# Kernel tuning notes

Hardware: AMD Instinct MI355X
Metric: run time of the kernel (lower is better)

Reference implementation:

```python
import jax, jax.numpy as jnp
import numpy as np

H = 128       # hidden size
IN = 6        # input size
OUT = 1       # output size
B, T = 128, 2048


def setup_inputs() -> dict:
    key = jax.random.key(0)
    ks = jax.random.split(key, 16)
    s = 1.0 / np.sqrt(H)  # PyTorch LSTM init: U(-1/sqrt(H), 1/sqrt(H))
    u = lambda k, shape: jax.random.uniform(k, shape, jnp.float32, -s, s)
    inp = {"x": jax.random.normal(ks[0], (B, T, IN), jnp.float32)}
    in_sizes = [IN, H, H]
    for l in range(3):
        inp[f"W_ih{l}"] = u(ks[1 + 4 * l], (4 * H, in_sizes[l]))
        inp[f"W_hh{l}"] = u(ks[2 + 4 * l], (4 * H, H))
        inp[f"b_ih{l}"] = u(ks[3 + 4 * l], (4 * H,))
        inp[f"b_hh{l}"] = u(ks[4 + 4 * l], (4 * H,))
    inp["W_out"] = u(ks[13], (OUT, H))
    inp["b_out"] = u(ks[14], (OUT,))
    return inp


def _lstm_layer(x, W_ih, W_hh, b):
    # x: [B, T, D_in]; precompute input contribution once, scan the recurrence.
    xg = jnp.einsum("bti,gi->btg", x, W_ih) + b  # [B, T, 4H]
    h0 = jnp.zeros((x.shape[0], H), x.dtype)
    c0 = jnp.zeros((x.shape[0], H), x.dtype)

    def step(carry, xg_t):
        h, c = carry
        g = xg_t + h @ W_hh.T                     # [B, 4H]
        i, f, gg, o = jnp.split(g, 4, axis=-1)    # PyTorch gate order i,f,g,o
        i = jax.nn.sigmoid(i)
        f = jax.nn.sigmoid(f)
        gg = jnp.tanh(gg)
        o = jax.nn.sigmoid(o)
        c = f * c + i * gg
        h = o * jnp.tanh(c)
        return (h, c), h

    _, hs = jax.lax.scan(step, (h0, c0), jnp.swapaxes(xg, 0, 1))  # hs: [T, B, H]
    return jnp.swapaxes(hs, 0, 1)


def reference(x, W_ih0, W_hh0, b_ih0, b_hh0, W_ih1, W_hh1, b_ih1, b_hh1,
              W_ih2, W_hh2, b_ih2, b_hh2, W_out, b_out):
    # 3-layer LSTM (dropout inactive in eval mode) + linear head on last step.
    h = _lstm_layer(x, W_ih0, W_hh0, b_ih0 + b_hh0)
    h = _lstm_layer(h, W_ih1, W_hh1, b_ih1 + b_hh1)
    h = _lstm_layer(h, W_ih2, W_hh2, b_ih2 + b_hh2)
    return h[:, -1, :] @ W_out.T + b_out  # [B, 1]
```

## Files before the change

### kernel.cpp

```cpp
#include <hip/hip_runtime.h>

#define B_ 128
#define T_ 2048
#define H_ 128
#define IN_ 6
#define GRP_ 8
#define NGRP_ (T_ / GRP_)
#define CHUNK_ 32
#define NCHUNK_ (T_ / CHUNK_)
#define FLAG_STRIDE_ 64
#define HS_ 144
#define XGRING_ 3
#define XGSLOT_ (CHUNK_ * 8192)
#define NSLICE_ 32
#define NFLAGS_ 144

typedef _Float16 f16x8 __attribute__((ext_vector_type(8)));
typedef float    f32x4 __attribute__((ext_vector_type(4)));

__device__ __forceinline__ unsigned short f2h_u(float f) {
  union { _Float16 h; unsigned short u; } v; v.h = (_Float16)f; return v.u;
}
__device__ __forceinline__ unsigned int pack2(float a, float b) {
  return (unsigned int)f2h_u(a) | ((unsigned int)f2h_u(b) << 16);
}
__device__ __forceinline__ float sigf_(float x) {
  return __builtin_amdgcn_rcpf(1.0f + __expf(-x));
}
__device__ __forceinline__ float tanhf_(float x) {
  return 2.0f * __builtin_amdgcn_rcpf(1.0f + __expf(-2.0f * x)) - 1.0f;
}
__device__ __forceinline__ f16x8 load_w8(const float* __restrict__ p) {
  f16x8 r;
#pragma unroll
  for (int i = 0; i < 8; ++i) r[i] = (_Float16)p[i];
  return r;
}

__global__ void init_flags(unsigned int* flags) {
  flags[blockIdx.x * 256 + threadIdx.x] = 0u;
}

#define BARRIER_LGKM()                                              \
  do {                                                              \
    asm volatile("s_waitcnt lgkmcnt(0)" ::: "memory");              \
    __builtin_amdgcn_s_barrier();                                   \
    __builtin_amdgcn_sched_barrier(0);                              \
  } while (0)

#define PUBLISH_FENCE()                                             \
  do {                                                              \
    asm volatile("s_waitcnt vmcnt(0)" ::: "memory");                \
    __builtin_amdgcn_s_barrier();                                   \
  } while (0)

__global__ __launch_bounds__(512, 2)
void lstm_pipe(const float* __restrict__ x,
               const float* __restrict__ Wih0, const float* __restrict__ Whh0,
               const float* __restrict__ bih0, const float* __restrict__ bhh0,
               const float* __restrict__ Wih1, const float* __restrict__ Whh1,
               const float* __restrict__ bih1, const float* __restrict__ bhh1,
               const float* __restrict__ Wih2, const float* __restrict__ Whh2,
               const float* __restrict__ bih2, const float* __restrict__ bhh2,
               unsigned short* __restrict__ region,
               float* __restrict__ xg,
               unsigned int* __restrict__ state_h,
               unsigned int* __restrict__ flags)
{
  const int bid  = blockIdx.x;
  const int tid  = threadIdx.x;
  const int lane = tid & 63;
  const int wv   = tid >> 6;
  const int n16  = lane & 15;
  const int quad = lane >> 4;

  __shared__ unsigned short smem[32 * 16 * HS_];
  __shared__ int s_have;

#define WAITP(ptr_, need_, have_)                                   \
  do {                                                              \
    if ((have_) < (need_)) {                                        \
      if (tid == 0) {                                               \
        int v = (int)__hip_atomic_load(ptr_, __ATOMIC_RELAXED,      \
                                       __HIP_MEMORY_SCOPE_AGENT);   \
        while (v < (need_)) {                                       \
          __builtin_amdgcn_s_sleep(2);                              \
          v = (int)__hip_atomic_load(ptr_, __ATOMIC_RELAXED,        \
                                     __HIP_MEMORY_SCOPE_AGENT);     \
        }                                                           \
        (void)__hip_atomic_load(ptr_, __ATOMIC_ACQUIRE,             \
                                __HIP_MEMORY_SCOPE_AGENT);          \
        s_have = v;                                                 \
      }                                                             \
      __syncthreads();                                              \
      (have_) = s_have;                                             \
    }                                                               \
  } while (0)

  if (bid >= 96) {
    const int gi = bid - 96;
    const int gl = 1 + (gi >> 3);
    const int bg = gi & 7;
    const int b8 = n16 & 7;
    const float* Wih = (gl == 1) ? Wih1 : Wih2;
    const float* bih = (gl == 1) ? bih1 : bih2;
    const float* bhh = (gl == 1) ? bhh1 : bhh2;
    float* xgo = xg + (size_t)((gl - 1) * 8 + bg) * (XGRING_ * (size_t)XGSLOT_);
    unsigned int* fhp[4]; unsigned int* fcp[4];
#pragma unroll
    for (int q = 0; q < 4; ++q) {
      fhp[q] = &flags[((gl - 1) * 32 + 4 * bg + q) * FLAG_STRIDE_];
      fcp[q] = &flags[(80 + (gl - 1) * 32 + 4 * bg + q) * FLAG_STRIDE_];
    }
    unsigned int* fx_out = &flags[(64 + (gl - 1) * 8 + bg) * FLAG_STRIDE_];

    f16x8 wih[4][4];
#pragma unroll
    for (int j = 0; j < 4; ++j)
#pragma unroll
      for (int kc = 0; kc < 4; ++kc)
        wih[j][kc] = load_w8(Wih + (size_t)(j * 128 + 16 * wv + n16) * H_ + kc * 32 + quad * 8);
    f32x4 bias4[4];
#pragma unroll
    for (int j = 0; j < 4; ++j)
#pragma unroll
      for (int r = 0; r < 4; ++r) {
        int row = j * 128 + 16 * wv + quad * 4 + r;
        bias4[j][r] = bih[row] + bhh[row];
      }

    int haveh0 = 0, haveh1 = 0, haveh2 = 0, haveh3 = 0;
    int havec0 = 0, havec1 = 0, havec2 = 0, havec3 = 0;
    const int tt = tid >> 4, bb = tid & 15;
    const int swk = bb & 7;
    for (int k = 0; k < NCHUNK_; ++k) {
      WAITP(fhp[0], k + 1, haveh0);
      WAITP(fhp[1], k + 1, haveh1);
      WAITP(fhp[2], k + 1, haveh2);
      WAITP(fhp[3], k + 1, haveh3);
      if (k >= XGRING_) {
        WAITP(fcp[0], k - (XGRING_ - 1), havec0);
        WAITP(fcp[1], k - (XGRING_ - 1), havec1);
        WAITP(fcp[2], k - (XGRING_ - 1), havec2);
        WAITP(fcp[3], k - (XGRING_ - 1), havec3);
      }
      {
        const uint4* gp = (const uint4*)(region +
            ((size_t)(bg * 16 + bb) * T_ + (size_t)(CHUNK_ * k + tt)) * H_);
        uint4* lp = (uint4*)&smem[(tt * 16 + bb) * HS_];
#pragma unroll
        for (int i = 0; i < 16; ++i) lp[i ^ swk] = gp[i];
      }
      __syncthreads();
      const int slot = k % XGRING_;
      for (int t = 0; t < CHUNK_; ++t) {
        f16x8 hi[4];
#pragma unroll
        for (int kc = 0; kc < 4; ++kc)
          hi[kc] = *(const f16x8*)&smem[(t * 16 + n16) * HS_ +
                                        ((kc * 32 + quad * 8) ^ (b8 << 3))];
        float* xp = xgo + (size_t)(slot * CHUNK_ + t) * 8192 + quad * 64 + n16 * 4;
#pragma unroll
        for (int j = 0; j < 4; ++j) {
          f32x4 a = bias4[j];
#pragma unroll
          for (int kc = 0; kc < 4; ++kc)
            a = __builtin_amdgcn_mfma_f32_16x16x32_f16(wih[j][kc], hi[kc], a, 0, 0, 0);
          *(f32x4*)(xp + (size_t)(8 * j + wv) * 256) = a;
        }
      }
      __syncthreads();
      if (tid == 0)
        __hip_atomic_store(fx_out, (unsigned int)(k + 1),
                           __ATOMIC_RELEASE, __HIP_MEMORY_SCOPE_AGENT);
    }
    return;
  }

  const int layer = bid >> 5;
  const int sl    = bid & 31;
  const int bcol  = n16 & 3;
  const int rr    = n16 >> 2;
  const int batch = sl * 4 + bcol;
  const float* Whh = (layer == 0) ? Whh0 : ((layer == 1) ? Whh1 : Whh2);

  unsigned short* hstate = smem;
  unsigned short* xb = smem + 2 * 4 * HS_;

  f16x8 whh[4][4];
#pragma unroll
  for (int j = 0; j < 4; ++j)
#pragma unroll
    for (int kc = 0; kc < 4; ++kc)
      whh[j][kc] = load_w8(Whh + (size_t)(j * 128 + 16 * wv + n16) * H_ + kc * 32 + quad * 8);

  for (int i = tid; i < (2 * 4 * HS_) / 2; i += 512) ((unsigned int*)smem)[i] = 0u;

  float cc_ = 0.f;
  unsigned short dh16[GRP_];
  const bool r2 = (rr & 2) != 0, r1 = (rr & 1) != 0;
  const int hcol = 16 * wv + 4 * quad + rr;
  const int s_i  = hcol;
  const int wswz = (((s_i >> 3) ^ bcol) << 3) | (s_i & 7);
  unsigned int* fh_out = (layer < 2) ? &flags[(layer * 32 + sl) * FLAG_STRIDE_] : nullptr;

  if (layer == 0) {
    f32x4 bias4[4];
#pragma unroll
    for (int j = 0; j < 4; ++j)
#pragma unroll
      for (int r = 0; r < 4; ++r) {
        int row = j * 128 + 16 * wv + quad * 4 + r;
        bias4[j][r] = bih0[row] + bhh0[row];
      }
    f16x8 wx[4];
#pragma unroll
    for (int j = 0; j < 4; ++j)
#pragma unroll
      for (int i = 0; i < 8; ++i) wx[j][i] = (_Float16)0.f;
    if (quad == 0) {
#pragma unroll
      for (int j = 0; j < 4; ++j) {
        const float* p = Wih0 + (size_t)(j * 128 + 16 * wv + n16) * IN_;
#pragma unroll
        for (int i = 0; i < IN_; ++i) wx[j][i] = (_Float16)p[i];
      }
    }
    const int sn_x = tid & 3, st_x = tid >> 2;
    float xraw[6];
    __syncthreads();
    if (tid < 32) {
      const float* xp = x + ((size_t)(sl * 4 + sn_x) * T_ + st_x) * IN_;
#pragma unroll
      for (int i = 0; i < IN_; ++i) xraw[i] = xp[i];
      uint4 xr4;
      xr4.x = pack2(xraw[0], xraw[1]); xr4.y = pack2(xraw[2], xraw[3]);
      xr4.z = pack2(xraw[4], xraw[5]); xr4.w = 0u;
      *(uint4*)&xb[(st_x * 4 + sn_x) * 8] = xr4;
    }
    __syncthreads();

    for (int g = 0; g < NGRP_; ++g) {
      if (tid < 32 && g + 1 < NGRP_) {
        const float* xp = x + ((size_t)(sl * 4 + sn_x) * T_ + (8 * (g + 1) + st_x)) * IN_;
#pragma unroll
        for (int i = 0; i < IN_; ++i) xraw[i] = xp[i];
      }
#pragma unroll
      for (int s = 0; s < GRP_; ++s) {
        const int rp = s & 1, wp = rp ^ 1;
        f16x8 hs[4];
#pragma unroll
        for (int kc = 0; kc < 4; ++kc)
          hs[kc] = *(const f16x8*)&hstate[(rp * 4 + bcol) * HS_ +
                                          ((kc * 32 + quad * 8) ^ (bcol << 3))];
        f16x8 xi;
#pragma unroll
        for (int i = 0; i < 8; ++i) xi[i] = (_Float16)0.f;
        if (quad == 0) xi = *(const f16x8*)&xb[(s * 4 + bcol) * 8];
        f32x4 acc[4];
#pragma unroll
        for (int j = 0; j < 4; ++j) {
          f32x4 a = __builtin_amdgcn_mfma_f32_16x16x32_f16(wx[j], xi, bias4[j], 0, 0, 0);
#pragma unroll
          for (int kc = 0; kc < 4; ++kc)
            a = __builtin_amdgcn_mfma_f32_16x16x32_f16(whh[j][kc], hs[kc], a, 0, 0, 0);
          acc[j] = a;
        }
        float g4[4];
#pragma unroll
        for (int j = 0; j < 4; ++j) {
          float t0 = r2 ? acc[j][2] : acc[j][0];
          float t1 = r2 ? acc[j][3] : acc[j][1];
          g4[j] = r1 ? t1 : t0;
        }
        float i_ = sigf_(g4[0]), f_ = sigf_(g4[1]), t_ = tanhf_(g4[2]), o_ = sigf_(g4[3]);
        cc_ = f_ * cc_ + i_ * t_;
        float h_ = o_ * tanhf_(cc_);
        unsigned short uh = f2h_u(h_);
        dh16[s] = uh;
        hstate[(wp * 4 + bcol) * HS_ + wswz] = uh;
        BARRIER_LGKM();
      }
#pragma unroll
      for (int s = 0; s < GRP_; ++s)
        region[((size_t)batch * T_ + (8 * g + s)) * H_ + hcol] = dh16[s];
      if (tid < 32 && g + 1 < NGRP_) {
        uint4 xr4;
        xr4.x = pack2(xraw[0], xraw[1]); xr4.y = pack2(xraw[2], xraw[3]);
        xr4.z = pack2(xraw[4], xraw[5]); xr4.w = 0u;
        *(uint4*)&xb[(st_x * 4 + sn_x) * 8] = xr4;
      }
      BARRIER_LGKM();
      if ((g & 3) == 3) {
        PUBLISH_FENCE();
        if (tid == 0)
          __hip_atomic_store(fh_out, (unsigned int)((g >> 2) + 1),
                             __ATOMIC_RELEASE, __HIP_MEMORY_SCOPE_AGENT);
      }
    }
  } else {
    const int bg = sl >> 2;
    const float* xgi = xg + (size_t)((layer - 1) * 8 + bg) * (XGRING_ * (size_t)XGSLOT_);
    const int xcol = (sl & 3) * 4 + bcol;
    f32x4 xr[2][4];
    auto load_xg = [&](int t, int buf) {
      int slot = (t >> 5) % XGRING_;
      const float* p = xgi + (size_t)(slot * CHUNK_ + (t & 31)) * 8192
                       + (size_t)wv * 256 + quad * 64 + xcol * 4;
      xr[buf][0] = *(const f32x4*)(p);
      xr[buf][1] = *(const f32x4*)(p + 2048);
      xr[buf][2] = *(const f32x4*)(p + 4096);
      xr[buf][3] = *(const f32x4*)(p + 6144);
    };
    unsigned int* fx_in  = &flags[(64 + (layer - 1) * 8 + bg) * FLAG_STRIDE_];
    unsigned int* fc_out = &flags[(80 + (layer - 1) * 32 + sl) * FLAG_STRIDE_];
    int have_x = 0;
    __syncthreads();

    for (int g = 0; g < NGRP_; ++g) {
      if ((g & 3) == 0) {
        int c = g >> 2;
        WAITP(fx_in, c + 1, have_x);
        load_xg(32 * c, 0);
        load_xg(32 * c + 1, 1);
      }
#pragma unroll
      for (int s = 0; s < GRP_; ++s) {
        const int t = 8 * g + s;
        const int rp = s & 1, wp = rp ^ 1;
        f16x8 hs[4];
#pragma unroll
        for (int kc = 0; kc < 4; ++kc)
          hs[kc] = *(const f16x8*)&hstate[(rp * 4 + bcol) * HS_ +
                                          ((kc * 32 + quad * 8) ^ (bcol << 3))];
        f32x4 ci[4];
#pragma unroll
        for (int j = 0; j < 4; ++j) ci[j] = xr[s & 1][j];
        if (!(((g & 3) == 3) && s >= 6)) load_xg(t + 2, s & 1);
        f32x4 acc[4];
#pragma unroll
        for (int j = 0; j < 4; ++j) {
          f32x4 a = ci[j];
#pragma unroll
          for (int kc = 0; kc < 4; ++kc)
            a = __builtin_amdgcn_mfma_f32_16x16x32_f16(whh[j][kc], hs[kc], a, 0, 0, 0);
          acc[j] = a;
        }
        float g4[4];
#pragma unroll
        for (int j = 0; j < 4; ++j) {
          float t0 = r2 ? acc[j][2] : acc[j][0];
          float t1 = r2 ? acc[j][3] : acc[j][1];
          g4[j] = r1 ? t1 : t0;
        }
        float i_ = sigf_(g4[0]), f_ = sigf_(g4[1]), t_ = tanhf_(g4[2]), o_ = sigf_(g4[3]);
        cc_ = f_ * cc_ + i_ * t_;
        float h_ = o_ * tanhf_(cc_);
        unsigned short uh = f2h_u(h_);
        dh16[s] = uh;
        hstate[(wp * 4 + bcol) * HS_ + wswz] = uh;
        BARRIER_LGKM();
      }
      if (layer == 1) {
#pragma unroll
        for (int s = 0; s < GRP_; ++s)
          region[((size_t)batch * T_ + (8 * g + s)) * H_ + hcol] = dh16[s];
      }
      if ((g & 3) == 3) {
        PUBLISH_FENCE();
        if (tid == 0) {
          unsigned int cdone = (unsigned int)((g >> 2) + 1);
          if (layer == 1)
            __hip_atomic_store(fh_out, cdone, __ATOMIC_RELEASE, __HIP_MEMORY_SCOPE_AGENT);
          __hip_atomic_store(fc_out, cdone, __ATOMIC_RELEASE, __HIP_MEMORY_SCOPE_AGENT);
        }
      }
    }
    if (layer == 2)
      ((unsigned short*)state_h)[(size_t)batch * 128 + hcol] = dh16[GRP_ - 1];
  }
#undef WAITP
}

__global__ void head_kernel(const unsigned int* __restrict__ state_h,
                            const float* __restrict__ Wout,
                            const float* __restrict__ bout,
                            float* __restrict__ out)
{
  int b = threadIdx.x;
  float s = bout[0];
  for (int j = 0; j < 64; ++j) {
    unsigned int p = state_h[b * 64 + j];
    union { unsigned short u; _Float16 h; } lo, hi;
    lo.u = (unsigned short)(p & 0xffffu);
    hi.u = (unsigned short)(p >> 16);
    s += (float)lo.h * Wout[2 * j] + (float)hi.h * Wout[2 * j + 1];
  }
  out[b] = s;
}

extern "C" void kernel_launch(void* const* d_in, const int* in_sizes, int n_in,
                              void* d_out, int out_size, void* d_ws, size_t ws_size,
                              hipStream_t stream)
{
  const float* x = (const float*)d_in[0];
  const float* Wih[3] = {(const float*)d_in[1], (const float*)d_in[5], (const float*)d_in[9]};
  const float* Whh[3] = {(const float*)d_in[2], (const float*)d_in[6], (const float*)d_in[10]};
  const float* bih[3] = {(const float*)d_in[3], (const float*)d_in[7], (const float*)d_in[11]};
  const float* bhh[3] = {(const float*)d_in[4], (const float*)d_in[8], (const float*)d_in[12]};
  const float* Wout = (const float*)d_in[13];
  const float* bout = (const float*)d_in[14];
  float* out = (float*)d_out;

  char* ws = (char*)d_ws;
  size_t off = 0;
  unsigned short* region = (unsigned short*)(ws + off); off += (size_t)B_ * T_ * H_ * 2;
  float* xg = (float*)(ws + off);                       off += (size_t)16 * XGRING_ * XGSLOT_ * 4;
  unsigned int* state_h  = (unsigned int*)(ws + off);   off += (size_t)B_ * 64 * 4;
  off = (off + 255) & ~(size_t)255;
  unsigned int* flags    = (unsigned int*)(ws + off);   off += NFLAGS_ * FLAG_STRIDE_ * 4;

  init_flags<<<36, 256, 0, stream>>>(flags);
  lstm_pipe<<<112, 512, 0, stream>>>(x,
      Wih[0], Whh[0], bih[0], bhh[0],
      Wih[1], Whh[1], bih[1], bhh[1],
      Wih[2], Whh[2], bih[2], bhh[2],
      region, xg, state_h, flags);
  head_kernel<<<1, 128, 0, stream>>>(state_h, Wout, bout, out);
}
```

Measured before the change: 1.541 ms.

## Split recurrent LSTM work across twice as many 256-thread blocks with two batches each

Result: slower. 1.925 ms (+24.9%).

```diff
diff --git a/kernel.cpp b/kernel.cpp
--- a/kernel.cpp
+++ b/kernel.cpp
@@ -12,8 +12,7 @@
 #define HS_ 144
 #define XGRING_ 3
 #define XGSLOT_ (CHUNK_ * 8192)
-#define NSLICE_ 32
-#define NFLAGS_ 144
+#define NFLAGS_ 272
 
 typedef _Float16 f16x8 __attribute__((ext_vector_type(8)));
 typedef float    f32x4 __attribute__((ext_vector_type(4)));
@@ -54,7 +53,7 @@
     __builtin_amdgcn_s_barrier();                                   \
   } while (0)
 
-__global__ __launch_bounds__(512, 2)
+__global__ __launch_bounds__(256, 1)
 void lstm_pipe(const float* __restrict__ x,
                const float* __restrict__ Wih0, const float* __restrict__ Whh0,
                const float* __restrict__ bih0, const float* __restrict__ bhh0,
@@ -97,8 +96,8 @@
     }                                                               \
   } while (0)
 
-  if (bid >= 96) {
-    const int gi = bid - 96;
+  if (bid >= 192) {
+    const int gi = bid - 192;
     const int gl = 1 + (gi >> 3);
     const int bg = gi & 7;
     const int b8 = n16 & 7;
@@ -106,45 +105,43 @@
     const float* bih = (gl == 1) ? bih1 : bih2;
     const float* bhh = (gl == 1) ? bhh1 : bhh2;
     float* xgo = xg + (size_t)((gl - 1) * 8 + bg) * (XGRING_ * (size_t)XGSLOT_);
-    unsigned int* fhp[4]; unsigned int* fcp[4];
-#pragma unroll
-    for (int q = 0; q < 4; ++q) {
-      fhp[q] = &flags[((gl - 1) * 32 + 4 * bg + q) * FLAG_STRIDE_];
-      fcp[q] = &flags[(80 + (gl - 1) * 32 + 4 * bg + q) * FLAG_STRIDE_];
-    }
-    unsigned int* fx_out = &flags[(64 + (gl - 1) * 8 + bg) * FLAG_STRIDE_];
-
-    f16x8 wih[4][4];
-#pragma unroll
-    for (int j = 0; j < 4; ++j)
+    unsigned int* fx_out = &flags[(128 + (gl - 1) * 8 + bg) * FLAG_STRIDE_];
+
+    f16x8 wih[8][4];
+#pragma unroll
+    for (int jp = 0; jp < 8; ++jp)
 #pragma unroll
       for (int kc = 0; kc < 4; ++kc)
-        wih[j][kc] = load_w8(Wih + (size_t)(j * 128 + 16 * wv + n16) * H_ + kc * 32 + quad * 8);
-    f32x4 bias4[4];
-#pragma unroll
-    for (int j = 0; j < 4; ++j)
+        wih[jp][kc] = load_w8(Wih + (size_t)((wv + 4 * jp) * 16 + n16) * H_ + kc * 32 + quad * 8);
+    f32x4 bias4[8];
+#pragma unroll
+    for (int jp = 0; jp < 8; ++jp)
 #pragma unroll
       for (int r = 0; r < 4; ++r) {
-        int row = j * 128 + 16 * wv + quad * 4 + r;
-        bias4[j][r] = bih[row] + bhh[row];
-      }
-
-    int haveh0 = 0, haveh1 = 0, haveh2 = 0, haveh3 = 0;
-    int havec0 = 0, havec1 = 0, havec2 = 0, havec3 = 0;
-    const int tt = tid >> 4, bb = tid & 15;
-    const int swk = bb & 7;
+        int row = (wv + 4 * jp) * 16 + quad * 4 + r;
+        bias4[jp][r] = bih[row] + bhh[row];
+      }
+
+    int have_h[8] = {0, 0, 0, 0, 0, 0, 0, 0};
+    int have_c[8] = {0, 0, 0, 0, 0, 0, 0, 0};
     for (int k = 0; k < NCHUNK_; ++k) {
-      WAITP(fhp[0], k + 1, haveh0);
-      WAITP(fhp[1], k + 1, haveh1);
-      WAITP(fhp[2], k + 1, haveh2);
-      WAITP(fhp[3], k + 1, haveh3);
+#pragma unroll
+      for (int q = 0; q < 8; ++q) {
+        unsigned int* fp = &flags[((gl - 1) * 64 + 8 * bg + q) * FLAG_STRIDE_];
+        WAITP(fp, k + 1, have_h[q]);
+      }
       if (k >= XGRING_) {
-        WAITP(fcp[0], k - (XGRING_ - 1), havec0);
-        WAITP(fcp[1], k - (XGRING_ - 1), havec1);
-        WAITP(fcp[2], k - (XGRING_ - 1), havec2);
-        WAITP(fcp[3], k - (XGRING_ - 1), havec3);
-      }
-      {
+#pragma unroll
+        for (int q = 0; q < 8; ++q) {
+          unsigned int* fp = &flags[(144 + (gl - 1) * 64 + 8 * bg + q) * FLAG_STRIDE_];
+          WAITP(fp, k - (XGRING_ - 1), have_c[q]);
+        }
+      }
+#pragma unroll
+      for (int rep = 0; rep < 2; ++rep) {
+        int row = tid + rep * 256;
+        int tt = row >> 4, bb = row & 15;
+        int swk = bb & 7;
         const uint4* gp = (const uint4*)(region +
             ((size_t)(bg * 16 + bb) * T_ + (size_t)(CHUNK_ * k + tt)) * H_);
         uint4* lp = (uint4*)&smem[(tt * 16 + bb) * HS_];
@@ -154,19 +151,19 @@
       __syncthreads();
       const int slot = k % XGRING_;
       for (int t = 0; t < CHUNK_; ++t) {
-        f16x8 hi[4];
+        f16x8 hi4[4];
 #pragma unroll
         for (int kc = 0; kc < 4; ++kc)
-          hi[kc] = *(const f16x8*)&smem[(t * 16 + n16) * HS_ +
-                                        ((kc * 32 + quad * 8) ^ (b8 << 3))];
+          hi4[kc] = *(const f16x8*)&smem[(t * 16 + n16) * HS_ +
+                                         ((kc * 32 + quad * 8) ^ (b8 << 3))];
         float* xp = xgo + (size_t)(slot * CHUNK_ + t) * 8192 + quad * 64 + n16 * 4;
 #pragma unroll
-        for (int j = 0; j < 4; ++j) {
-          f32x4 a = bias4[j];
+        for (int jp = 0; jp < 8; ++jp) {
+          f32x4 a = bias4[jp];
 #pragma unroll
           for (int kc = 0; kc < 4; ++kc)
-            a = __builtin_amdgcn_mfma_f32_16x16x32_f16(wih[j][kc], hi[kc], a, 0, 0, 0);
-          *(f32x4*)(xp + (size_t)(8 * j + wv) * 256) = a;
+            a = __builtin_amdgcn_mfma_f32_16x16x32_f16(wih[jp][kc], hi4[kc], a, 0, 0, 0);
+          *(f32x4*)(xp + (size_t)(wv + 4 * jp) * 256) = a;
         }
       }
       __syncthreads();
@@ -177,72 +174,71 @@
     return;
   }
 
-  const int layer = bid >> 5;
-  const int sl    = bid & 31;
-  const int bcol  = n16 & 3;
-  const int rr    = n16 >> 2;
-  const int batch = sl * 4 + bcol;
+  const int layer = bid >> 6;
+  const int sl    = bid & 63;
+  const int bcol  = n16 & 1;
+  const int hib   = (n16 >> 1) & 1;
+  const int rsel  = n16 >> 2;
+  const bool r1   = (rsel & 1) != 0, rr2 = (rsel & 2) != 0;
+  const int batch = sl * 2 + bcol;
+  const int hcol  = 16 * wv + 64 * hib + 4 * quad + rsel;
   const float* Whh = (layer == 0) ? Whh0 : ((layer == 1) ? Whh1 : Whh2);
 
   unsigned short* hstate = smem;
-  unsigned short* xb = smem + 2 * 4 * HS_;
-
-  f16x8 whh[4][4];
-#pragma unroll
-  for (int j = 0; j < 4; ++j)
+  unsigned short* xb = smem + 2 * 2 * HS_;
+
+  f16x8 whh[8][4];
+#pragma unroll
+  for (int jj = 0; jj < 8; ++jj)
 #pragma unroll
     for (int kc = 0; kc < 4; ++kc)
-      whh[j][kc] = load_w8(Whh + (size_t)(j * 128 + 16 * wv + n16) * H_ + kc * 32 + quad * 8);
-
-  for (int i = tid; i < (2 * 4 * HS_) / 2; i += 512) ((unsigned int*)smem)[i] = 0u;
+      whh[jj][kc] = load_w8(Whh + (size_t)((wv + 4 * jj) * 16 + n16) * H_ + kc * 32 + quad * 8);
+
+  for (int i = tid; i < (2 * 2 * HS_) / 2; i += 256) ((unsigned int*)smem)[i] = 0u;
 
   float cc_ = 0.f;
   unsigned short dh16[GRP_];
-  const bool r2 = (rr & 2) != 0, r1 = (rr & 1) != 0;
-  const int hcol = 16 * wv + 4 * quad + rr;
-  const int s_i  = hcol;
-  const int wswz = (((s_i >> 3) ^ bcol) << 3) | (s_i & 7);
-  unsigned int* fh_out = (layer < 2) ? &flags[(layer * 32 + sl) * FLAG_STRIDE_] : nullptr;
+  unsigned int* fh_out = (layer < 2) ? &flags[(layer * 64 + sl) * FLAG_STRIDE_] : nullptr;
 
   if (layer == 0) {
-    f32x4 bias4[4];
-#pragma unroll
-    for (int j = 0; j < 4; ++j)
+    f32x4 bias4[8];
+#pragma unroll
+    for (int jj = 0; jj < 8; ++jj)
 #pragma unroll
       for (int r = 0; r < 4; ++r) {
-        int row = j * 128 + 16 * wv + quad * 4 + r;
-        bias4[j][r] = bih0[row] + bhh0[row];
-      }
-    f16x8 wx[4];
-#pragma unroll
-    for (int j = 0; j < 4; ++j)
-#pragma unroll
-      for (int i = 0; i < 8; ++i) wx[j][i] = (_Float16)0.f;
+        int row = (wv + 4 * jj) * 16 + quad * 4 + r;
+        bias4[jj][r] = bih0[row] + bhh0[row];
+      }
+    f16x8 wx[8];
+#pragma unroll
+    for (int jj = 0; jj < 8; ++jj)
+#pragma unroll
+      for (int i = 0; i < 8; ++i) wx[jj][i] = (_Float16)0.f;
     if (quad == 0) {
 #pragma unroll
-      for (int j = 0; j < 4; ++j) {
-        const float* p = Wih0 + (size_t)(j * 128 + 16 * wv + n16) * IN_;
-#pragma unroll
-        for (int i = 0; i < IN_; ++i) wx[j][i] = (_Float16)p[i];
+      for (int jj = 0; jj < 8; ++jj) {
+        const float* p = Wih0 + (size_t)((wv + 4 * jj) * 16 + n16) * IN_;
+#pragma unroll
+        for (int i = 0; i < IN_; ++i) wx[jj][i] = (_Float16)p[i];
       }
     }
-    const int sn_x = tid & 3, st_x = tid >> 2;
+    const int sn_x = tid & 1, st_x = tid >> 1;
     float xraw[6];
     __syncthreads();
-    if (tid < 32) {
-      const float* xp = x + ((size_t)(sl * 4 + sn_x) * T_ + st_x) * IN_;
+    if (tid < 16) {
+      const float* xp = x + ((size_t)(sl * 2 + sn_x) * T_ + st_x) * IN_;
 #pragma unroll
       for (int i = 0; i < IN_; ++i) xraw[i] = xp[i];
       uint4 xr4;
       xr4.x = pack2(xraw[0], xraw[1]); xr4.y = pack2(xraw[2], xraw[3]);
       xr4.z = pack2(xraw[4], xraw[5]); xr4.w = 0u;
-      *(uint4*)&xb[(st_x * 4 + sn_x) * 8] = xr4;
+      *(uint4*)&xb[(st_x * 2 + sn_x) * 8] = xr4;
     }
     __syncthreads();
 
     for (int g = 0; g < NGRP_; ++g) {
-      if (tid < 32 && g + 1 < NGRP_) {
-        const float* xp = x + ((size_t)(sl * 4 + sn_x) * T_ + (8 * (g + 1) + st_x)) * IN_;
+      if (tid < 16 && g + 1 < NGRP_) {
+        const float* xp = x + ((size_t)(sl * 2 + sn_x) * T_ + (8 * (g + 1) + st_x)) * IN_;
 #pragma unroll
         for (int i = 0; i < IN_; ++i) xraw[i] = xp[i];
       }
@@ -252,44 +248,46 @@
         f16x8 hs[4];
 #pragma unroll
         for (int kc = 0; kc < 4; ++kc)
-          hs[kc] = *(const f16x8*)&hstate[(rp * 4 + bcol) * HS_ +
-                                          ((kc * 32 + quad * 8) ^ (bcol << 3))];
+          hs[kc] = *(const f16x8*)&hstate[(rp * 2 + bcol) * HS_ + kc * 32 + quad * 8];
         f16x8 xi;
 #pragma unroll
         for (int i = 0; i < 8; ++i) xi[i] = (_Float16)0.f;
-        if (quad == 0) xi = *(const f16x8*)&xb[(s * 4 + bcol) * 8];
-        f32x4 acc[4];
+        if (quad == 0) xi = *(const f16x8*)&xb[(s * 2 + bcol) * 8];
+        f32x4 acc[8];
+#pragma unroll
+        for (int jj = 0; jj < 8; ++jj)
+          acc[jj] = __builtin_amdgcn_mfma_f32_16x16x32_f16(wx[jj], xi, bias4[jj], 0, 0, 0);
+#pragma unroll
+        for (int kc = 0; kc < 4; ++kc)
+#pragma unroll
+          for (int jj = 0; jj < 8; ++jj)
+            acc[jj] = __builtin_amdgcn_mfma_f32_16x16x32_f16(whh[jj][kc], hs[kc], acc[jj], 0, 0, 0);
+        float g4[4];
 #pragma unroll
         for (int j = 0; j < 4; ++j) {
-          f32x4 a = __builtin_amdgcn_mfma_f32_16x16x32_f16(wx[j], xi, bias4[j], 0, 0, 0);
-#pragma unroll
-          for (int kc = 0; kc < 4; ++kc)
-            a = __builtin_amdgcn_mfma_f32_16x16x32_f16(whh[j][kc], hs[kc], a, 0, 0, 0);
-          acc[j] = a;
-        }
-        float g4[4];
-#pragma unroll
-        for (int j = 0; j < 4; ++j) {
-          float t0 = r2 ? acc[j][2] : acc[j][0];
-          float t1 = r2 ? acc[j][3] : acc[j][1];
-          g4[j] = r1 ? t1 : t0;
+          f32x4 va;
+#pragma unroll
+          for (int r = 0; r < 4; ++r) va[r] = hib ? acc[2 * j + 1][r] : acc[2 * j][r];
+          float t0 = r1 ? va[1] : va[0];
+          float t1 = r1 ? va[3] : va[2];
+          g4[j] = rr2 ? t1 : t0;
         }
         float i_ = sigf_(g4[0]), f_ = sigf_(g4[1]), t_ = tanhf_(g4[2]), o_ = sigf_(g4[3]);
         cc_ = f_ * cc_ + i_ * t_;
         float h_ = o_ * tanhf_(cc_);
         unsigned short uh = f2h_u(h_);
         dh16[s] = uh;
-        hstate[(wp * 4 + bcol) * HS_ + wswz] = uh;
+        hstate[(wp * 2 + bcol) * HS_ + hcol] = uh;
         BARRIER_LGKM();
       }
 #pragma unroll
       for (int s = 0; s < GRP_; ++s)
         region[((size_t)batch * T_ + (8 * g + s)) * H_ + hcol] = dh16[s];
-      if (tid < 32 && g + 1 < NGRP_) {
+      if (tid < 16 && g + 1 < NGRP_) {
         uint4 xr4;
         xr4.x = pack2(xraw[0], xraw[1]); xr4.y = pack2(xraw[2], xraw[3]);
         xr4.z = pack2(xraw[4], xraw[5]); xr4.w = 0u;
-        *(uint4*)&xb[(st_x * 4 + sn_x) * 8] = xr4;
+        *(uint4*)&xb[(st_x * 2 + sn_x) * 8] = xr4;
       }
       BARRIER_LGKM();
       if ((g & 3) == 3) {
@@ -300,21 +298,20 @@
       }
     }
   } else {
-    const int bg = sl >> 2;
+    const int bg = sl >> 3;
     const float* xgi = xg + (size_t)((layer - 1) * 8 + bg) * (XGRING_ * (size_t)XGSLOT_);
-    const int xcol = (sl & 3) * 4 + bcol;
-    f32x4 xr[2][4];
+    const int xcol = (sl & 7) * 2 + bcol;
+    f32x4 xr[2][8];
     auto load_xg = [&](int t, int buf) {
       int slot = (t >> 5) % XGRING_;
       const float* p = xgi + (size_t)(slot * CHUNK_ + (t & 31)) * 8192
-                       + (size_t)wv * 256 + quad * 64 + xcol * 4;
-      xr[buf][0] = *(const f32x4*)(p);
-      xr[buf][1] = *(const f32x4*)(p + 2048);
-      xr[buf][2] = *(const f32x4*)(p + 4096);
-      xr[buf][3] = *(const f32x4*)(p + 6144);
+                       + quad * 64 + xcol * 4;
+#pragma unroll
+      for (int jj = 0; jj < 8; ++jj)
+        xr[buf][jj] = *(const f32x4*)(p + (size_t)(wv + 4 * jj) * 256);
     };
-    unsigned int* fx_in  = &flags[(64 + (layer - 1) * 8 + bg) * FLAG_STRIDE_];
-    unsigned int* fc_out = &flags[(80 + (layer - 1) * 32 + sl) * FLAG_STRIDE_];
+    unsigned int* fx_in  = &flags[(128 + (layer - 1) * 8 + bg) * FLAG_STRIDE_];
+    unsigned int* fc_out = &flags[(144 + (layer - 1) * 64 + sl) * FLAG_STRIDE_];
     int have_x = 0;
     __syncthreads();
 
@@ -332,34 +329,33 @@
         f16x8 hs[4];
 #pragma unroll
         for (int kc = 0; kc < 4; ++kc)
-          hs[kc] = *(const f16x8*)&hstate[(rp * 4 + bcol) * HS_ +
-                                          ((kc * 32 + quad * 8) ^ (bcol << 3))];
-        f32x4 ci[4];
-#pragma unroll
-        for (int j = 0; j < 4; ++j) ci[j] = xr[s & 1][j];
+          hs[kc] = *(const f16x8*)&hstate[(rp * 2 + bcol) * HS_ + kc * 32 + quad * 8];
+        f32x4 acc[8];
+#pragma unroll
+        for (int jj = 0; jj < 8; ++jj)
+          acc[jj] = __builtin_amdgcn_mfma_f32_16x16x32_f16(whh[jj][0], hs[0], xr[s & 1][jj], 0, 0, 0);
         if (!(((g & 3) == 3) && s >= 6)) load_xg(t + 2, s & 1);
-        f32x4 acc[4];
+#pragma unroll
+        for (int kc = 1; kc < 4; ++kc)
+#pragma unroll
+          for (int jj = 0; jj < 8; ++jj)
+            acc[jj] = __builtin_amdgcn_mfma_f32_16x16x32_f16(whh[jj][kc], hs[kc], acc[jj], 0, 0, 0);
+        float g4[4];
 #pragma unroll
         for (int j = 0; j < 4; ++j) {
-          f32x4 a = ci[j];
-#pragma unroll
-          for (int kc = 0; kc < 4; ++kc)
-            a = __builtin_amdgcn_mfma_f32_16x16x32_f16(whh[j][kc], hs[kc], a, 0, 0, 0);
-          acc[j] = a;
-        }
-        float g4[4];
-#pragma unroll
-        for (int j = 0; j < 4; ++j) {
-          float t0 = r2 ? acc[j][2] : acc[j][0];
-          float t1 = r2 ? acc[j][3] : acc[j][1];
-          g4[j] = r1 ? t1 : t0;
+          f32x4 va;
+#pragma unroll
+          for (int r = 0; r < 4; ++r) va[r] = hib ? acc[2 * j + 1][r] : acc[2 * j][r];
+          float t0 = r1 ? va[1] : va[0];
+          float t1 = r1 ? va[3] : va[2];
+          g4[j] = rr2 ? t1 : t0;
         }
         float i_ = sigf_(g4[0]), f_ = sigf_(g4[1]), t_ = tanhf_(g4[2]), o_ = sigf_(g4[3]);
         cc_ = f_ * cc_ + i_ * t_;
         float h_ = o_ * tanhf_(cc_);
         unsigned short uh = f2h_u(h_);
         dh16[s] = uh;
-        hstate[(wp * 4 + bcol) * HS_ + wswz] = uh;
+        hstate[(wp * 2 + bcol) * HS_ + hcol] = uh;
         BARRIER_LGKM();
       }
       if (layer == 1) {
@@ -421,8 +417,8 @@
   off = (off + 255) & ~(size_t)255;
   unsigned int* flags    = (unsigned int*)(ws + off);   off += NFLAGS_ * FLAG_STRIDE_ * 4;
 
-  init_flags<<<36, 256, 0, stream>>>(flags);
-  lstm_pipe<<<112, 512, 0, stream>>>(x,
+  init_flags<<<68, 256, 0, stream>>>(flags);
+  lstm_pipe<<<208, 256, 0, stream>>>(x,
       Wih[0], Whh[0], bih[0], bhh[0],
       Wih[1], Whh[1], bih[1], bhh[1],
       Wih[2], Whh[2], bih[2], bhh[2],
```
